# Performance work log

Hardware: AMD Instinct MI355X
Metric: run time of the kernel (lower is better)

## Reference

```python
import jax, jax.numpy as jnp
import numpy as np

B, S, E, H = 4, 2048, 1024, 16
D = E // H  # head_size = 64


def setup_inputs() -> dict:
    key = jax.random.key(0)
    ks = jax.random.split(key, 5)
    x = jax.random.normal(ks[0], (B, S, E), dtype=jnp.float32)
    # nn.Linear default init ~ U(-1/sqrt(fan_in), 1/sqrt(fan_in))
    bound = 1.0 / np.sqrt(E)
    W_qkv = jax.random.uniform(ks[1], (E, 3 * E), dtype=jnp.float32, minval=-bound, maxval=bound)
    b_qkv = jax.random.uniform(ks[2], (3 * E,), dtype=jnp.float32, minval=-bound, maxval=bound)
    W_out = jax.random.uniform(ks[3], (E, E), dtype=jnp.float32, minval=-bound, maxval=bound)
    b_out = jax.random.uniform(ks[4], (E,), dtype=jnp.float32, minval=-bound, maxval=bound)
    return {"x": x, "W_qkv": W_qkv, "b_qkv": b_qkv, "W_out": W_out, "b_out": b_out, "mask": 1}


def reference(x, W_qkv, b_qkv, W_out, b_out, mask):
    qkv = x @ W_qkv + b_qkv                              # [B,S,3E]
    qkv = qkv.reshape(B, S, H, 3 * D).transpose(0, 2, 1, 3)  # [B,H,S,3D]
    q, k, v = jnp.split(qkv, 3, axis=-1)                  # each [B,H,S,D]
    scale = 1.0 / np.sqrt(E)  # NOTE: original divides by sqrt(n_embd), not sqrt(head_size)
    y = jnp.einsum('bhqd,bhkd->bhqk', q, k) * scale       # [B,H,S,S]
    if mask:
        causal = jnp.tril(jnp.ones((S, S), dtype=bool))
        y = jnp.where(causal, y, -1e9)
    y = jax.nn.softmax(y, axis=-1)
    vals = jnp.einsum('bhqk,bhkd->bhqd', y, v)            # [B,H,S,D]
    vals = vals.transpose(0, 2, 1, 3).reshape(B, S, E)
    return vals @ W_out + b_out
```

## Files before the change

kernel.cpp:

```cpp
#include <hip/hip_runtime.h>
#include <hip/hip_bf16.h>
#include <cstdint>
#include <cstddef>

typedef __bf16 bf16;
typedef __bf16 bf16x8 __attribute__((ext_vector_type(8)));
typedef float f32x4 __attribute__((ext_vector_type(4)));
typedef unsigned int u32x4 __attribute__((ext_vector_type(4)));
typedef unsigned int u32x2 __attribute__((ext_vector_type(2)));

#define DEVINL __device__ __forceinline__

namespace {
constexpr int Bb = 4, Ss = 2048, Ee = 1024, Hh = 16;
constexpr int Mm = Bb * Ss;
constexpr int N_QKV = 3 * Ee;
constexpr float SCQ = 0.03125f * 1.44269504f;
}

DEVINL void gl_lds16(const bf16* g, bf16* l) {
  __builtin_amdgcn_global_load_lds((const __attribute__((address_space(1))) void*)g,
                                   (__attribute__((address_space(3))) void*)l, 16, 0, 0);
}

DEVINL unsigned int pkbf(float a, float b) {
  bf16 x = (bf16)a, y = (bf16)b;
  return (unsigned int)__builtin_bit_cast(unsigned short, x) |
         ((unsigned int)__builtin_bit_cast(unsigned short, y) << 16);
}


__global__ void k_cvt_bf16(const float* __restrict__ in, bf16* __restrict__ out, int n) {
  int i = (blockIdx.x * 256 + threadIdx.x) * 8;
  if (i >= n) return;
  float4 a = *(const float4*)(in + i);
  float4 c = *(const float4*)(in + i + 4);
  bf16x8 v = {(bf16)a.x, (bf16)a.y, (bf16)a.z, (bf16)a.w,
              (bf16)c.x, (bf16)c.y, (bf16)c.z, (bf16)c.w};
  *(bf16x8*)(out + i) = v;
}

__global__ void k_transpose_cvt(const float* __restrict__ in, bf16* __restrict__ out, int R, int C) {
  __shared__ float tile[32][33];
  const int c0 = blockIdx.x * 32, r0 = blockIdx.y * 32;
  const int tx = threadIdx.x, ty = threadIdx.y;
  for (int i = 0; i < 32; i += 8)
    tile[ty + i][tx] = in[(size_t)(r0 + ty + i) * C + (c0 + tx)];
  __syncthreads();
  for (int i = 0; i < 32; i += 8)
    out[(size_t)(c0 + ty + i) * R + (r0 + tx)] = (bf16)tile[tx][ty + i];
}


template <int NF>
DEVINL void gemm_core256(const bf16* __restrict__ A, const bf16* __restrict__ Bt,
                         int m0, int n0, bf16* As, bf16* Bs, f32x4 (&acc)[8][NF]) {
  constexpr int K = 1024;
  constexpr int TILEA = 16384;
  constexpr int TILEB = NF * 4096;
  const int tid = threadIdx.x;
  const int w = tid >> 6, lane = tid & 63;
  const int wm = w >> 2, wn = w & 3;
  const int fr = lane & 15, kg = lane >> 4;
  const int gc = (tid & 7) ^ ((tid >> 3) & 7);
  const int srow = tid >> 3;
  const bf16* Ag = A + (size_t)(m0 + srow) * K + gc * 8;
  const bf16* Bg = Bt + (size_t)(n0 + srow) * K + gc * 8;
  bf16* AdW = As + w * 512;
  bf16* BdW = Bs + w * 512;

#define STAGE_TILE(kt, buf)                                                       \
  {                                                                               \
    for (int i = 0; i < 4; ++i)                                                   \
      gl_lds16(Ag + (kt) + (size_t)(i * 64) * K, AdW + (buf) * TILEA + i * 4096); \
    for (int i = 0; i < NF; ++i)                                                  \
      gl_lds16(Bg + (kt) + (size_t)(i * 64) * K, BdW + (buf) * TILEB + i * 4096); \
  }

  STAGE_TILE(0, 0)
  STAGE_TILE(64, 1)
  constexpr int nt = K / 64;
  for (int t = 0; t < nt; ++t) {
    const int cur = t & 1;
    if constexpr (NF == 3) {
      asm volatile("s_waitcnt vmcnt(7)" ::: "memory");
    } else {
      asm volatile("s_waitcnt vmcnt(6)" ::: "memory");
    }
    __builtin_amdgcn_sched_barrier(0);
    __builtin_amdgcn_s_barrier();
    __builtin_amdgcn_sched_barrier(0);
    bf16x8 af[2][8], bfx[2][NF];
    const bf16* Ab = As + cur * TILEA;
    const bf16* Bb = Bs + cur * TILEB;
    for (int kk = 0; kk < 2; ++kk) {
      const int sw = ((kk * 4 + kg) ^ (fr & 7)) * 8;
      for (int mi = 0; mi < 8; ++mi)
        af[kk][mi] = *(const bf16x8*)(Ab + (wm * 128 + mi * 16 + fr) * 64 + sw);
      for (int ni = 0; ni < NF; ++ni)
        bfx[kk][ni] = *(const bf16x8*)(Bb + (wn * (NF * 16) + ni * 16 + fr) * 64 + sw);
    }
    asm volatile("s_waitcnt lgkmcnt(0)" ::: "memory");
    __builtin_amdgcn_sched_barrier(0);
    __builtin_amdgcn_s_barrier();
    __builtin_amdgcn_sched_barrier(0);
    if (t + 2 < nt) STAGE_TILE((t + 2) * 64, cur)
    __builtin_amdgcn_s_setprio(1);
    for (int kk = 0; kk < 2; ++kk)
      for (int mi = 0; mi < 8; ++mi)
        for (int ni = 0; ni < NF; ++ni)
          acc[mi][ni] =
              __builtin_amdgcn_mfma_f32_16x16x32_bf16(af[kk][mi], bfx[kk][ni], acc[mi][ni], 0, 0, 0);
    __builtin_amdgcn_s_setprio(0);
  }
#undef STAGE_TILE
}

__global__ __launch_bounds__(512, 2) void k_qkv_gemm(const bf16* __restrict__ A,
                                                     const bf16* __restrict__ Bt,
                                                     const float* __restrict__ bias,
                                                     bf16* __restrict__ qbuf,
                                                     bf16* __restrict__ kbuf,
                                                     bf16* __restrict__ vtb) {
  __shared__ bf16 As[2 * 16384];
  __shared__ bf16 Bs[2 * 3 * 4096];
  const int m0 = blockIdx.y * 256, n0 = blockIdx.x * 192;
  f32x4 acc[8][3] = {};
  gemm_core256<3>(A, Bt, m0, n0, As, Bs, acc);

  const int tid = threadIdx.x, w = tid >> 6, lane = tid & 63;
  const int wm = w >> 2, wn = w & 3;
  const int fr = lane & 15, kg = lane >> 4;
  const int row_b = m0 >> 11;
  for (int ni = 0; ni < 3; ++ni) {
    const int col0 = n0 + wn * 48 + ni * 16;
    const int h = col0 / 192;
    const int w192 = col0 - h * 192;
    const int cls = w192 >> 6;
    const float bv = bias[col0 + fr];
    if (cls == 2) {
      const int d = w192 - 128 + fr;
      bf16* dstb = vtb + (((size_t)row_b * Hh + h) * 64 + d) * Ss;
      for (int mi = 0; mi < 8; ++mi) {
        const int s0 = (m0 & 2047) + wm * 128 + mi * 16 + kg * 4;
        u32x2 pk2 = {pkbf(acc[mi][ni][0] + bv, acc[mi][ni][1] + bv),
                     pkbf(acc[mi][ni][2] + bv, acc[mi][ni][3] + bv)};
        *(u32x2*)(dstb + s0) = pk2;
      }
    } else {
      bf16* buf = (cls == 0) ? qbuf : kbuf;
      const float sc = (cls == 0) ? SCQ : 1.f;
      const int d = (w192 & 63) + fr;
      bf16* dstb = buf + ((size_t)row_b * Hh + h) * Ss * 64 + d;
      for (int mi = 0; mi < 8; ++mi) {
        const int s0 = (m0 & 2047) + wm * 128 + mi * 16 + kg * 4;
        for (int r = 0; r < 4; ++r)
          dstb[(size_t)(s0 + r) * 64] = (bf16)((acc[mi][ni][r] + bv) * sc);
      }
    }
  }
}

__global__ __launch_bounds__(512, 2) void k_out_gemm(const bf16* __restrict__ A,
                                                     const bf16* __restrict__ Bt,
                                                     const float* __restrict__ bias,
                                                     float* __restrict__ out) {
  __shared__ bf16 As[2 * 16384];
  __shared__ bf16 Bs[2 * 2 * 4096];
  const int m0 = blockIdx.y * 256, n0 = blockIdx.x * 128;
  f32x4 acc[8][2] = {};
  gemm_core256<2>(A, Bt, m0, n0, As, Bs, acc);

  const int tid = threadIdx.x, w = tid >> 6, lane = tid & 63;
  const int wm = w >> 2, wn = w & 3;
  const int fr = lane & 15, kg = lane >> 4;
  for (int ni = 0; ni < 2; ++ni) {
    const int col = n0 + wn * 32 + ni * 16 + fr;
    const float bv = bias[col];
    for (int mi = 0; mi < 8; ++mi) {
      const int mb = m0 + wm * 128 + mi * 16 + kg * 4;
      for (int r = 0; r < 4; ++r)
        out[(size_t)(mb + r) * Ee + col] = acc[mi][ni][r] + bv;
    }
  }
}


__global__ __launch_bounds__(256, 3) void k_attn(const bf16* __restrict__ qbuf,
                                                 const bf16* __restrict__ kbuf,
                                                 const bf16* __restrict__ vtb,
                                                 bf16* __restrict__ vals) {
  const int g = blockIdx.x;
  const int qt = 15 - (g >> 6);
  const int bh = g & 63;
  const int b = bh >> 4, h = bh & 15;
  const int q0 = qt * 128;
  const int tid = threadIdx.x, w = tid >> 6, lane = tid & 63;
  const int fr = lane & 15, kg = lane >> 4;
  const int rl = lane >> 3, cl = (lane & 7) ^ (lane >> 3);

  __shared__ bf16 KsB[2][4096];
  __shared__ bf16 VtB[2][4096];

  const bf16* qb = qbuf + (size_t)bh * Ss * 64;
  const bf16* kb = kbuf + (size_t)bh * Ss * 64 + (size_t)rl * 64 + cl * 8;
  const bf16* vb = vtb + (size_t)bh * 64 * Ss + (size_t)rl * Ss + cl * 8;

  const int gA = (kg & 1) * 32 + fr;
  const int gB = gA + 16;
  const bool hiSel = (kg >> 1) != 0;

  bf16x8 aq[2][2];
  for (int sub = 0; sub < 2; ++sub) {
    const bf16* qr = qb + (size_t)(q0 + w * 32 + sub * 16 + fr) * 64 + kg * 8;
    aq[sub][0] = *(const bf16x8*)(qr);
    aq[sub][1] = *(const bf16x8*)(qr + 32);
  }

  float m_run[2] = {-1e30f, -1e30f}, l_run[2] = {0.f, 0.f};
  f32x4 o_acc[2][4] = {};

  const int nt = 2 * qt + 2;

  for (int t = 0; t < 2; ++t) {
    const int i = w * 2 + t;
    gl_lds16(kb + (size_t)(i * 8) * 64, KsB[0] + i * 512);
    gl_lds16(vb + (size_t)(i * 8) * Ss, VtB[0] + i * 512);
  }

  int cur = 0;
  for (int it = 0; it < nt; ++it) {
    const int kv0 = it * 64;
    __syncthreads();
    if (it + 1 < nt) {
      const int kvn = kv0 + 64;
      for (int t = 0; t < 2; ++t) {
        const int i = w * 2 + t;
        gl_lds16(kb + (size_t)(kvn + i * 8) * 64, KsB[cur ^ 1] + i * 512);
        gl_lds16(vb + (size_t)(i * 8) * Ss + kvn, VtB[cur ^ 1] + i * 512);
      }
    }
    const bool active = (kv0 <= q0 + w * 32 + 31);
    if (active) {
      f32x4 sacc[2][4] = {};
      for (int kk = 0; kk < 2; ++kk) {
        bf16x8 bk[4];
        for (int ni = 0; ni < 4; ++ni) {
          const int rb = ni * 16 + fr;
          bk[ni] = *(const bf16x8*)(KsB[cur] + rb * 64 + (((kk * 4 + kg) ^ (rb & 7)) * 8));
        }
        __builtin_amdgcn_s_setprio(1);
        for (int sub = 0; sub < 2; ++sub)
          for (int ni = 0; ni < 4; ++ni)
            sacc[sub][ni] =
                __builtin_amdgcn_mfma_f32_16x16x32_bf16(bk[ni], aq[sub][kk], sacc[sub][ni], 0, 0, 0);
        __builtin_amdgcn_s_setprio(0);
      }
      bf16x8 bp[2][2];
      for (int sub = 0; sub < 2; ++sub) {
        const int qs = q0 + w * 32 + sub * 16;
        float p[4][4];
        float mnew = -1e30f;
        if (kv0 + 63 > qs) {
          const int q = qs + fr;
          for (int ni = 0; ni < 4; ++ni)
            for (int r = 0; r < 4; ++r) {
              const int k = kv0 + ni * 16 + kg * 4 + r;
              float s = sacc[sub][ni][r];
              if (k > q) s = -1e30f;
              p[ni][r] = s;
              mnew = fmaxf(mnew, s);
            }
        } else {
          for (int ni = 0; ni < 4; ++ni)
            for (int r = 0; r < 4; ++r) {
              float s = sacc[sub][ni][r];
              p[ni][r] = s;
              mnew = fmaxf(mnew, s);
            }
        }
        mnew = fmaxf(mnew, __shfl_xor(mnew, 16, 64));
        mnew = fmaxf(mnew, __shfl_xor(mnew, 32, 64));
        float mn;
        if (__all(mnew - m_run[sub] <= 8.f)) {
          mn = m_run[sub];
        } else {
          mn = fmaxf(m_run[sub], mnew);
          const float fs = exp2f(m_run[sub] - mn);
          m_run[sub] = mn;
          l_run[sub] *= fs;
          for (int ni = 0; ni < 4; ++ni)
            for (int r = 0; r < 4; ++r)
              o_acc[sub][ni][r] *= fs;
        }
        float rs = 0.f;
        for (int ni = 0; ni < 4; ++ni)
          for (int r = 0; r < 4; ++r) {
            const float e = exp2f(p[ni][r] - mn);
            p[ni][r] = e;
            rs += e;
          }
        rs += __shfl_xor(rs, 16, 64);
        rs += __shfl_xor(rs, 32, 64);
        l_run[sub] += rs;
        unsigned int Wlo[4], Whi[4];
        for (int ni = 0; ni < 4; ++ni) {
          Wlo[ni] = pkbf(p[ni][0], p[ni][1]);
          Whi[ni] = pkbf(p[ni][2], p[ni][3]);
        }
        for (int kk = 0; kk < 2; ++kk) {
          const int i0 = 2 * kk, i1 = 2 * kk + 1;
          unsigned int a0 = (unsigned int)__shfl((int)Wlo[i0], gA, 64);
          unsigned int a1 = (unsigned int)__shfl((int)Wlo[i1], gA, 64);
          unsigned int b0 = (unsigned int)__shfl((int)Whi[i0], gA, 64);
          unsigned int b1 = (unsigned int)__shfl((int)Whi[i1], gA, 64);
          unsigned int c0 = (unsigned int)__shfl((int)Wlo[i0], gB, 64);
          unsigned int c1 = (unsigned int)__shfl((int)Wlo[i1], gB, 64);
          unsigned int d0 = (unsigned int)__shfl((int)Whi[i0], gB, 64);
          unsigned int d1 = (unsigned int)__shfl((int)Whi[i1], gB, 64);
          u32x4 wv = {hiSel ? a1 : a0, hiSel ? b1 : b0, hiSel ? c1 : c0, hiSel ? d1 : d0};
          bp[sub][kk] = __builtin_bit_cast(bf16x8, wv);
        }
      }
      for (int kk = 0; kk < 2; ++kk) {
        bf16x8 bv[4];
        for (int ni = 0; ni < 4; ++ni) {
          const int rb = ni * 16 + fr;
          bv[ni] = *(const bf16x8*)(VtB[cur] + rb * 64 + (((kk * 4 + kg) ^ (rb & 7)) * 8));
        }
        __builtin_amdgcn_s_setprio(1);
        for (int sub = 0; sub < 2; ++sub)
          for (int ni = 0; ni < 4; ++ni)
            o_acc[sub][ni] =
                __builtin_amdgcn_mfma_f32_16x16x32_bf16(bv[ni], bp[sub][kk], o_acc[sub][ni], 0, 0, 0);
        __builtin_amdgcn_s_setprio(0);
      }
    }
    cur ^= 1;
  }

  for (int sub = 0; sub < 2; ++sub) {
    const float inv = 1.f / l_run[sub];
    const int q = q0 + w * 32 + sub * 16 + fr;
    bf16* dst = vals + ((size_t)b * Ss + q) * Ee + h * 64 + kg * 4;
    for (int ni = 0; ni < 4; ++ni) {
      u32x2 pk2 = {pkbf(o_acc[sub][ni][0] * inv, o_acc[sub][ni][1] * inv),
                   pkbf(o_acc[sub][ni][2] * inv, o_acc[sub][ni][3] * inv)};
      *(u32x2*)(dst + ni * 16) = pk2;
    }
  }
}


extern "C" void kernel_launch(void* const* d_in, const int* in_sizes, int n_in,
                              void* d_out, int out_size, void* d_ws, size_t ws_size,
                              hipStream_t stream) {
  const float* x    = (const float*)d_in[0];
  const float* Wqkv = (const float*)d_in[1];
  const float* bqkv = (const float*)d_in[2];
  const float* Wout = (const float*)d_in[3];
  const float* bout = (const float*)d_in[4];
  float* out = (float*)d_out;

  char* ws = (char*)d_ws;
  const size_t MiB = 1048576, KiB = 1024;
  bf16* x_bf  = (bf16*)(ws);
  bf16* valsb = (bf16*)(ws);
  bf16* WqkvT = (bf16*)(ws + 16 * MiB);
  bf16* WoutT = (bf16*)(ws + 22 * MiB);
  bf16* qbuf  = (bf16*)(ws + 24 * MiB);
  bf16* kbuf  = (bf16*)(ws + 40 * MiB + 192 * KiB);
  bf16* vtb   = (bf16*)(ws + 56 * MiB + 384 * KiB);

  k_cvt_bf16<<<dim3(Mm * Ee / 2048), dim3(256), 0, stream>>>(x, x_bf, Mm * Ee);
  k_transpose_cvt<<<dim3(N_QKV / 32, Ee / 32), dim3(32, 8), 0, stream>>>(Wqkv, WqkvT, Ee, N_QKV);
  k_transpose_cvt<<<dim3(Ee / 32, Ee / 32), dim3(32, 8), 0, stream>>>(Wout, WoutT, Ee, Ee);
  k_qkv_gemm<<<dim3(N_QKV / 192, Mm / 256), dim3(512), 0, stream>>>(x_bf, WqkvT, bqkv, qbuf, kbuf, vtb);
  k_attn<<<dim3(Ss / 128 * Hh * Bb), dim3(256), 0, stream>>>(qbuf, kbuf, vtb, valsb);
  k_out_gemm<<<dim3(Ee / 128, Mm / 256), dim3(512), 0, stream>>>(valsb, WoutT, bout, out);
}
```

Before: 191.3 us.

## Use triple-buffered LDS pipeline with one barrier per k-step in GEMMs

Replaces the double-buffered GEMM core with a three-stage LDS ring, so the next tile load is issued right after a single barrier instead of after a second barrier following the LDS reads. Both GEMMs now use 256x128 tiles, so the QKV GEMM drops from 192-wide to 128-wide N tiles and launches more blocks. The aim is to remove one barrier per iteration and overlap global loads with compute more deeply. In exchange LDS use per block rises to 144 KiB, which could limit two blocks per CU, and the narrower QKV tile re-reads A more often.

```diff
diff --git a/kernel.cpp b/kernel.cpp
--- a/kernel.cpp
+++ b/kernel.cpp
@@ -52,12 +52,11 @@
 }
 
 
-template <int NF>
-DEVINL void gemm_core256(const bf16* __restrict__ A, const bf16* __restrict__ Bt,
-                         int m0, int n0, bf16* As, bf16* Bs, f32x4 (&acc)[8][NF]) {
+DEVINL void gemm_core3(const bf16* __restrict__ A, const bf16* __restrict__ Bt,
+                       int m0, int n0, bf16* As, bf16* Bs, f32x4 (&acc)[8][2]) {
   constexpr int K = 1024;
   constexpr int TILEA = 16384;
-  constexpr int TILEB = NF * 4096;
+  constexpr int TILEB = 8192;
   const int tid = threadIdx.x;
   const int w = tid >> 6, lane = tid & 63;
   const int wm = w >> 2, wn = w & 3;
@@ -73,45 +72,45 @@
   {                                                                               \
     for (int i = 0; i < 4; ++i)                                                   \
       gl_lds16(Ag + (kt) + (size_t)(i * 64) * K, AdW + (buf) * TILEA + i * 4096); \
-    for (int i = 0; i < NF; ++i)                                                  \
+    for (int i = 0; i < 2; ++i)                                                   \
       gl_lds16(Bg + (kt) + (size_t)(i * 64) * K, BdW + (buf) * TILEB + i * 4096); \
   }
 
   STAGE_TILE(0, 0)
   STAGE_TILE(64, 1)
   constexpr int nt = K / 64;
+  int cur = 0, sb = 2;
+#pragma unroll 1
   for (int t = 0; t < nt; ++t) {
-    const int cur = t & 1;
-    if constexpr (NF == 3) {
-      asm volatile("s_waitcnt vmcnt(7)" ::: "memory");
+    if (t != nt - 1) {
+      asm volatile("s_waitcnt vmcnt(6) lgkmcnt(0)" ::: "memory");
     } else {
-      asm volatile("s_waitcnt vmcnt(6)" ::: "memory");
+      asm volatile("s_waitcnt vmcnt(0) lgkmcnt(0)" ::: "memory");
     }
     __builtin_amdgcn_sched_barrier(0);
     __builtin_amdgcn_s_barrier();
     __builtin_amdgcn_sched_barrier(0);
-    bf16x8 af[2][8], bfx[2][NF];
+    if (t + 2 < nt) STAGE_TILE((t + 2) * 64, sb)
+    __builtin_amdgcn_sched_barrier(0);
+    bf16x8 af[2][8], bfx[2][2];
     const bf16* Ab = As + cur * TILEA;
     const bf16* Bb = Bs + cur * TILEB;
     for (int kk = 0; kk < 2; ++kk) {
       const int sw = ((kk * 4 + kg) ^ (fr & 7)) * 8;
       for (int mi = 0; mi < 8; ++mi)
         af[kk][mi] = *(const bf16x8*)(Ab + (wm * 128 + mi * 16 + fr) * 64 + sw);
-      for (int ni = 0; ni < NF; ++ni)
-        bfx[kk][ni] = *(const bf16x8*)(Bb + (wn * (NF * 16) + ni * 16 + fr) * 64 + sw);
-    }
-    asm volatile("s_waitcnt lgkmcnt(0)" ::: "memory");
-    __builtin_amdgcn_sched_barrier(0);
-    __builtin_amdgcn_s_barrier();
-    __builtin_amdgcn_sched_barrier(0);
-    if (t + 2 < nt) STAGE_TILE((t + 2) * 64, cur)
+      for (int ni = 0; ni < 2; ++ni)
+        bfx[kk][ni] = *(const bf16x8*)(Bb + (wn * 32 + ni * 16 + fr) * 64 + sw);
+    }
     __builtin_amdgcn_s_setprio(1);
     for (int kk = 0; kk < 2; ++kk)
       for (int mi = 0; mi < 8; ++mi)
-        for (int ni = 0; ni < NF; ++ni)
+        for (int ni = 0; ni < 2; ++ni)
           acc[mi][ni] =
               __builtin_amdgcn_mfma_f32_16x16x32_bf16(af[kk][mi], bfx[kk][ni], acc[mi][ni], 0, 0, 0);
     __builtin_amdgcn_s_setprio(0);
+    cur = (cur == 2) ? 0 : cur + 1;
+    sb = (sb == 2) ? 0 : sb + 1;
   }
 #undef STAGE_TILE
 }
@@ -122,18 +121,18 @@
                                                      bf16* __restrict__ qbuf,
                                                      bf16* __restrict__ kbuf,
                                                      bf16* __restrict__ vtb) {
-  __shared__ bf16 As[2 * 16384];
-  __shared__ bf16 Bs[2 * 3 * 4096];
-  const int m0 = blockIdx.y * 256, n0 = blockIdx.x * 192;
-  f32x4 acc[8][3] = {};
-  gemm_core256<3>(A, Bt, m0, n0, As, Bs, acc);
+  __shared__ bf16 As[3 * 16384];
+  __shared__ bf16 Bs[3 * 8192];
+  const int m0 = blockIdx.y * 256, n0 = blockIdx.x * 128;
+  f32x4 acc[8][2] = {};
+  gemm_core3(A, Bt, m0, n0, As, Bs, acc);
 
   const int tid = threadIdx.x, w = tid >> 6, lane = tid & 63;
   const int wm = w >> 2, wn = w & 3;
   const int fr = lane & 15, kg = lane >> 4;
   const int row_b = m0 >> 11;
-  for (int ni = 0; ni < 3; ++ni) {
-    const int col0 = n0 + wn * 48 + ni * 16;
+  for (int ni = 0; ni < 2; ++ni) {
+    const int col0 = n0 + wn * 32 + ni * 16;
     const int h = col0 / 192;
     const int w192 = col0 - h * 192;
     const int cls = w192 >> 6;
@@ -165,11 +164,11 @@
                                                      const bf16* __restrict__ Bt,
                                                      const float* __restrict__ bias,
                                                      float* __restrict__ out) {
-  __shared__ bf16 As[2 * 16384];
-  __shared__ bf16 Bs[2 * 2 * 4096];
+  __shared__ bf16 As[3 * 16384];
+  __shared__ bf16 Bs[3 * 8192];
   const int m0 = blockIdx.y * 256, n0 = blockIdx.x * 128;
   f32x4 acc[8][2] = {};
-  gemm_core256<2>(A, Bt, m0, n0, As, Bs, acc);
+  gemm_core3(A, Bt, m0, n0, As, Bs, acc);
 
   const int tid = threadIdx.x, w = tid >> 6, lane = tid & 63;
   const int wm = w >> 2, wn = w & 3;
@@ -375,7 +374,7 @@
   k_cvt_bf16<<<dim3(Mm * Ee / 2048), dim3(256), 0, stream>>>(x, x_bf, Mm * Ee);
   k_transpose_cvt<<<dim3(N_QKV / 32, Ee / 32), dim3(32, 8), 0, stream>>>(Wqkv, WqkvT, Ee, N_QKV);
   k_transpose_cvt<<<dim3(Ee / 32, Ee / 32), dim3(32, 8), 0, stream>>>(Wout, WoutT, Ee, Ee);
-  k_qkv_gemm<<<dim3(N_QKV / 192, Mm / 256), dim3(512), 0, stream>>>(x_bf, WqkvT, bqkv, qbuf, kbuf, vtb);
+  k_qkv_gemm<<<dim3(N_QKV / 128, Mm / 256), dim3(512), 0, stream>>>(x_bf, WqkvT, bqkv, qbuf, kbuf, vtb);
   k_attn<<<dim3(Ss / 128 * Hh * Bb), dim3(256), 0, stream>>>(qbuf, kbuf, vtb, valsb);
   k_out_gemm<<<dim3(Ee / 128, Mm / 256), dim3(512), 0, stream>>>(valsb, WoutT, bout, out);
 }
```

New measurement: 206.2 us. 1.08x slower.
